# Kernel tuning notes

Measured on AMD Instinct MI355X. Metric: run time of the kernel, lower is better.

The kernel has to match this reference:

```python
import jax, jax.numpy as jnp
import numpy as np

B, N, M = 2, 4096, 1024
QD, CD, H, DH = 512, 768, 8, 64
SCALE = DH ** -0.5


def setup_inputs() -> dict:
    key = jax.random.key(0)
    ks = jax.random.split(key, 8)
    return {
        "x": jax.random.normal(ks[0], (B, N, QD), jnp.float32),
        "context": jax.random.normal(ks[1], (B, M, CD), jnp.float32),
        "adapt": jax.random.normal(ks[2], (B, N, H * DH), jnp.float32),
        "Wq": jax.random.normal(ks[3], (QD, H * DH), jnp.float32) * (QD ** -0.5),
        "Wk": jax.random.normal(ks[4], (CD, H * DH), jnp.float32) * (CD ** -0.5),
        "Wv": jax.random.normal(ks[5], (CD, H * DH), jnp.float32) * (CD ** -0.5),
        "Wo": jax.random.normal(ks[6], (H * DH, QD), jnp.float32) * ((H * DH) ** -0.5),
        "bo": jnp.zeros((QD,), jnp.float32),
    }


def _split_heads(t):
    # [b, n, h*d] -> [b, h, n, d]
    b, n, _ = t.shape
    return t.reshape(b, n, H, DH).transpose(0, 2, 1, 3)


def reference(x, context, adapt, Wq, Wk, Wv, Wo, bo):
    q = _split_heads(x @ Wq)          # [b,h,n,d]
    k = _split_heads(context @ Wk)    # [b,h,m,d]
    v = _split_heads(context @ Wv)    # [b,h,m,d]

    sim = jnp.einsum('bhid,bhjd->bhij', q, k) * SCALE  # [b,h,n,m]
    attn = jax.nn.softmax(sim, axis=-1)
    # NOTE: module averages raw logits (sim) over heads, not softmax probs
    attention_probs_avg = sim.mean(axis=1)             # [b,n,m]
    out = jnp.einsum('bhij,bhjd->bhid', attn, v)       # [b,h,n,d]

    # adapt-query pass reusing k, v
    qa = _split_heads(adapt)
    sim_a = jnp.einsum('bhid,bhjd->bhij', qa, k) * SCALE
    attn_a = jax.nn.softmax(sim_a, axis=-1)
    out = out + jnp.einsum('bhij,bhjd->bhid', attn_a, v)

    out = out.transpose(0, 2, 1, 3).reshape(B, N, H * DH)  # merge heads
    return (out @ Wo + bo, attention_probs_avg)
```

## Files before the change

### kernel.cpp

```cpp
#include <hip/hip_runtime.h>

typedef __attribute__((ext_vector_type(8))) short bh8;
typedef __attribute__((ext_vector_type(4))) float f4;
typedef __attribute__((ext_vector_type(4))) unsigned short us4;
typedef __attribute__((ext_vector_type(4))) unsigned int u32x4;

__device__ __forceinline__ unsigned short rne_bf16(float x) {
  unsigned int u = __builtin_bit_cast(unsigned int, x);
  u += 0x7fffu + ((u >> 16) & 1u);
  return (unsigned short)(u >> 16);
}

__device__ __forceinline__ unsigned int cvt_pk_bf16(float lo, float hi) {
  unsigned int r;
  asm("v_cvt_pk_bf16_f32 %0, %1, %2" : "=v"(r) : "v"(lo), "v"(hi));
  return r;
}

__device__ __forceinline__ void gl_lds16(const void* g, void* l) {
  __builtin_amdgcn_global_load_lds(
      (const __attribute__((address_space(1))) void*)g,
      (__attribute__((address_space(3))) void*)l, 16, 0, 0);
}

__global__ __launch_bounds__(256) void prep_kernel(
    const float* __restrict__ x, unsigned short* __restrict__ xb,
    const float* __restrict__ context, unsigned short* __restrict__ cb,
    const float* __restrict__ Wq, const float* __restrict__ Wk,
    const float* __restrict__ Wv, const float* __restrict__ Wo,
    unsigned short* __restrict__ WqT, unsigned short* __restrict__ WkvT,
    unsigned short* __restrict__ WoT) {
  const int bid = blockIdx.x, tid = threadIdx.x;
  if (bid < 1024) {
    const int n40 = (8192 * 512) / 4, n41 = (2048 * 768) / 4;
    const int total = n40 + n41, stride = 1024 * 256;
    for (int i = bid * 256 + tid; i < total; i += stride) {
      const float* in = (i < n40) ? x : context;
      unsigned short* out = (i < n40) ? xb : cb;
      const int j = (i < n40) ? i : (i - n40);
      f4 v = *(const f4*)(in + (long)j * 4);
      us4 o;
#pragma unroll
      for (int e = 0; e < 4; ++e) o[e] = rne_bf16(v[e]);
      *(us4*)(out + (long)j * 4) = o;
    }
    return;
  }
  int u = bid - 1024;
  const float* in;
  unsigned short* out;
  int K;
  if (u < 256)       { in = Wq; out = WqT;               K = 512; }
  else if (u < 640)  { u -= 256; in = Wk; out = WkvT;    K = 768; }
  else if (u < 1024) { u -= 640; in = Wv; out = WkvT + 512L * 768; K = 768; }
  else               { u -= 1024; in = Wo; out = WoT;    K = 512; }
  const int N = 512;
  const int n0 = (u & 15) * 32, k0 = (u >> 4) * 32;
  __shared__ float t[32][33];
  const int tx = tid & 31, ty = tid >> 5;
#pragma unroll
  for (int r = 0; r < 32; r += 8)
    t[ty + r][tx] = in[(long)(k0 + ty + r) * N + n0 + tx];
  __syncthreads();
#pragma unroll
  for (int r = 0; r < 32; r += 8)
    out[(long)(n0 + ty + r) * K + k0 + tx] = rne_bf16(t[tx][ty + r]);
}

__global__ __launch_bounds__(256) void vt_kernel(
    const unsigned short* __restrict__ KVb, unsigned short* __restrict__ VTb) {
  const int u = blockIdx.x;
  const int j0 = (u & 63) * 32, d0 = (u >> 6) * 32;
  __shared__ unsigned short t[32][34];
  const int tx = threadIdx.x & 31, ty = threadIdx.x >> 5;
#pragma unroll
  for (int r = 0; r < 32; r += 8)
    t[ty + r][tx] = KVb[(long)(j0 + ty + r) * 1024 + 512 + d0 + tx];
  __syncthreads();
#pragma unroll
  for (int r = 0; r < 32; r += 8)
    VTb[(long)(d0 + ty + r) * 2048 + j0 + tx] = t[tx][ty + r];
}

template <int MODE>
__device__ __forceinline__ void gemm_body(
    char* ldsb,
    const unsigned short* __restrict__ A, const unsigned short* __restrict__ Bt,
    void* __restrict__ Cv, int K, int lda, int ldb, int ldc,
    long astr, long bstr, long cstr, float scale, const float* __restrict__ bias,
    int bx, int by, int bz) {
  char* Asb = ldsb;
  char* Bsb = ldsb + 32768;
  const int tid = threadIdx.x, w = tid >> 6, l = tid & 63;
  const int c = l & 15, g = l >> 4;
  const int m0 = by * 128, n0 = bx * 128;
  const unsigned short* Ab = A + (long)bz * astr;
  const unsigned short* Bb = Bt + (long)bz * bstr;

  auto stage = [&](int buf, int kt) {
#pragma unroll
    for (int s = 0; s < 4; ++s) {
      const int idx = w * 4 + s;
      const int row = ((idx >> 1) & 7) * 16 + c;
      const int col = kt * 64 + (idx & 1) * 32 + g * 8;
      gl_lds16(Ab + (long)(m0 + row) * lda + col, Asb + buf * 16384 + idx * 1024);
      gl_lds16(Bb + (long)(n0 + row) * ldb + col, Bsb + buf * 16384 + idx * 1024);
    }
  };

  f4 acc[4][4];
#pragma unroll
  for (int i = 0; i < 4; ++i)
#pragma unroll
    for (int j = 0; j < 4; ++j) acc[i][j] = (f4){0.f, 0.f, 0.f, 0.f};

  const int nkt = K >> 6;
  stage(0, 0);
  asm volatile("s_waitcnt vmcnt(0)" ::: "memory");
  __syncthreads();

  for (int kt = 0; kt < nkt; ++kt) {
    const int cur = kt & 1;
    if (kt + 1 < nkt) stage(cur ^ 1, kt + 1);
#pragma unroll
    for (int kk = 0; kk < 2; ++kk) {
      bh8 af[4], bfr[4];
#pragma unroll
      for (int i = 0; i < 4; ++i) {
        af[i] = *(const bh8*)(Asb + cur * 16384 + (((w >> 1) * 8 + i * 2 + kk) * 1024) + l * 16);
        bfr[i] = *(const bh8*)(Bsb + cur * 16384 + (((w & 1) * 8 + i * 2 + kk) * 1024) + l * 16);
      }
#pragma unroll
      for (int i = 0; i < 4; ++i)
#pragma unroll
        for (int j = 0; j < 4; ++j)
          acc[i][j] = __builtin_amdgcn_mfma_f32_16x16x32_bf16(af[i], bfr[j], acc[i][j], 0, 0, 0);
    }
    if (kt + 1 < nkt) {
      asm volatile("s_waitcnt vmcnt(0)" ::: "memory");
      __syncthreads();
    }
  }

  const int rbase = m0 + (w >> 1) * 64, cbase = n0 + (w & 1) * 64;
#pragma unroll
  for (int i = 0; i < 4; ++i)
#pragma unroll
    for (int j = 0; j < 4; ++j)
#pragma unroll
      for (int r = 0; r < 4; ++r) {
        const long row = rbase + i * 16 + g * 4 + r;
        const long col = cbase + j * 16 + c;
        const float v = acc[i][j][r];
        if (MODE == 0) {
          ((unsigned short*)Cv + (long)bz * cstr)[row * ldc + col] = rne_bf16(v * scale);
        } else if (MODE == 1) {
          ((float*)Cv + (long)bz * cstr)[row * ldc + col] = v * scale;
        } else {
          ((float*)Cv)[row * ldc + col] = v + bias[col];
        }
      }
}

template <int MODE>
__device__ __forceinline__ void gemm_body64(
    char* ldsb,
    const unsigned short* __restrict__ A, const unsigned short* __restrict__ Bt,
    void* __restrict__ Cv, int K, int lda, int ldb, int ldc,
    float scale, const float* __restrict__ bias, int bx, int by) {
  char* Asb = ldsb;
  char* Bsb = ldsb + 32768;
  const int tid = threadIdx.x, w = tid >> 6, l = tid & 63;
  const int c = l & 15, g = l >> 4;
  const int m0 = by * 128, n0 = bx * 64;
  const int wr = w & 1, wc = w >> 1;

  auto stage = [&](int buf, int kt) {
#pragma unroll
    for (int s = 0; s < 6; ++s) {
      const int idx = w * 6 + s;
      if (idx < 16) {
        const int row = (idx >> 1) * 16 + c;
        const int col = kt * 64 + (idx & 1) * 32 + g * 8;
        gl_lds16(A + (long)(m0 + row) * lda + col, Asb + buf * 16384 + idx * 1024);
      } else {
        const int ib = idx - 16;
        const int row = (ib >> 1) * 16 + c;
        const int col = kt * 64 + (ib & 1) * 32 + g * 8;
        gl_lds16(Bt + (long)(n0 + row) * ldb + col, Bsb + buf * 8192 + ib * 1024);
      }
    }
  };

  f4 acc[4][2];
#pragma unroll
  for (int i = 0; i < 4; ++i)
#pragma unroll
    for (int j = 0; j < 2; ++j) acc[i][j] = (f4){0.f, 0.f, 0.f, 0.f};

  const int nkt = K >> 6;
  stage(0, 0);
  asm volatile("s_waitcnt vmcnt(0)" ::: "memory");
  __syncthreads();

  for (int kt = 0; kt < nkt; ++kt) {
    const int cur = kt & 1;
    if (kt + 1 < nkt) stage(cur ^ 1, kt + 1);
#pragma unroll
    for (int kk = 0; kk < 2; ++kk) {
      bh8 af[4], bfr[2];
#pragma unroll
      for (int i = 0; i < 4; ++i)
        af[i] = *(const bh8*)(Asb + cur * 16384 + (((wr * 4 + i) * 2 + kk) * 1024) + l * 16);
#pragma unroll
      for (int j = 0; j < 2; ++j)
        bfr[j] = *(const bh8*)(Bsb + cur * 8192 + (((wc * 2 + j) * 2 + kk) * 1024) + l * 16);
#pragma unroll
      for (int i = 0; i < 4; ++i)
#pragma unroll
        for (int j = 0; j < 2; ++j)
          acc[i][j] = __builtin_amdgcn_mfma_f32_16x16x32_bf16(af[i], bfr[j], acc[i][j], 0, 0, 0);
    }
    if (kt + 1 < nkt) {
      asm volatile("s_waitcnt vmcnt(0)" ::: "memory");
      __syncthreads();
    }
  }

  const int rbase = m0 + wr * 64, cbase = n0 + wc * 32;
#pragma unroll
  for (int i = 0; i < 4; ++i)
#pragma unroll
    for (int j = 0; j < 2; ++j)
#pragma unroll
      for (int r = 0; r < 4; ++r) {
        const long row = rbase + i * 16 + g * 4 + r;
        const long col = cbase + j * 16 + c;
        const float v = acc[i][j][r];
        if (MODE == 0) {
          ((unsigned short*)Cv)[row * ldc + col] = rne_bf16(v * scale);
        } else if (MODE == 2) {
          ((float*)Cv)[row * ldc + col] = v + bias[col];
        }
      }
}

__global__ __launch_bounds__(256, 3) void gemm_qkv(
    const unsigned short* __restrict__ xb, const unsigned short* __restrict__ WqT,
    unsigned short* __restrict__ Qb,
    const unsigned short* __restrict__ cb, const unsigned short* __restrict__ WkvT,
    unsigned short* __restrict__ KVb, float cexp) {
  __shared__ char lds[49152];
  const int bid = blockIdx.x;
  const unsigned short *A, *Bt;
  unsigned short* C;
  int K, ldb_, ldc_, bx, by;
  float sc;
  if (bid < 512) {
    A = xb; Bt = WqT; C = Qb; K = 512; ldb_ = 512; ldc_ = 512;
    bx = bid & 7; by = bid >> 3; sc = cexp;
  } else {
    const int u = bid - 512;
    A = cb; Bt = WkvT; C = KVb; K = 768; ldb_ = 768; ldc_ = 1024;
    bx = u & 15; by = u >> 4; sc = 1.f;
  }
  gemm_body64<0>(lds, A, Bt, C, K, K, ldb_, ldc_, sc, nullptr, bx, by);
}

__global__ __launch_bounds__(256, 2) void final_kernel(
    const unsigned short* __restrict__ Qb, const unsigned short* __restrict__ KVb,
    float* __restrict__ out1, float avg_scale,
    const unsigned short* __restrict__ Ob, const unsigned short* __restrict__ WoT,
    float* __restrict__ out0, const float* __restrict__ bias) {
  extern __shared__ char lds[];
  const int bid = blockIdx.x;
  if (bid < 512) {
    gemm_body<1>(lds, Qb, KVb, out1, 512, 512, 1024, 1024,
                 4096L * 512, 1024L * 1024, 4096L * 1024, avg_scale, nullptr,
                 bid & 7, (bid >> 3) & 31, bid >> 8);
  } else {
    const int u = bid - 512;
    gemm_body64<2>(lds, Ob, WoT, out0, 512, 512, 512, 512, 1.f, bias, u & 7, u >> 3);
  }
}

__global__ __launch_bounds__(256, 4) void attn_kernel(
    const unsigned short* __restrict__ Qb, const float* __restrict__ adapt,
    const unsigned short* __restrict__ KV, const unsigned short* __restrict__ VT,
    unsigned short* __restrict__ Ob) {
  __shared__ unsigned short Ks[2][8 * 512];
  __shared__ unsigned short Vs[2][8 * 512];
  const int qt = blockIdx.y, h = blockIdx.x, b = blockIdx.z;
  const int tid = threadIdx.x, w = tid >> 6, l = tid & 63;
  const int c = l & 15, g = l >> 4;
  const float CEXP = 0.18033688011112042f;

  const unsigned short* Kg = KV + ((long)b * 1024) * 1024 + h * 64;
  const unsigned short* Vg = VT + (long)h * 64 * 2048 + b * 1024;

  auto stage = [&](int buf, int jt0) {
#pragma unroll
    for (int s = 0; s < 2; ++s) {
      const int idx = w * 2 + s;
      const int row = (idx >> 1) * 16 + c;
      const int col = (idx & 1) * 32 + g * 8;
      gl_lds16(Kg + ((long)jt0 * 64 + row) * 1024 + col, (char*)&Ks[buf][0] + idx * 1024);
      gl_lds16(Vg + (long)row * 2048 + jt0 * 64 + col, (char*)&Vs[buf][0] + idx * 1024);
    }
  };

  stage(0, 0);

  const long qrow = (long)b * 4096 + qt * 64 + w * 16 + c;
  bh8 qf[2][2];
#pragma unroll
  for (int kk = 0; kk < 2; ++kk) {
    const int col = h * 64 + kk * 32 + g * 8;
    qf[0][kk] = *(const bh8*)(Qb + qrow * 512 + col);
    const float* ap = adapt + qrow * 512 + col;
    f4 x0 = *(const f4*)ap, x1 = *(const f4*)(ap + 4);
    bh8 t;
#pragma unroll
    for (int e = 0; e < 4; ++e) {
      t[e] = (short)rne_bf16(x0[e] * CEXP);
      t[e + 4] = (short)rne_bf16(x1[e] * CEXP);
    }
    qf[1][kk] = t;
  }

  const u32x4 ones_u = {0x3F803F80u, 0x3F803F80u, 0x3F803F80u, 0x3F803F80u};
  const bh8 ones = __builtin_bit_cast(bh8, ones_u);

  f4 psacc[2];
  f4 accv[2][4];
#pragma unroll
  for (int qs = 0; qs < 2; ++qs) {
    psacc[qs] = (f4){0.f, 0.f, 0.f, 0.f};
#pragma unroll
    for (int dt = 0; dt < 4; ++dt) accv[qs][dt] = (f4){0.f, 0.f, 0.f, 0.f};
  }

  asm volatile("s_waitcnt vmcnt(0)" ::: "memory");
  __syncthreads();

  auto make_pf = [&](const f4& s2k, const f4& s2k1) -> bh8 {
    unsigned int p0 = cvt_pk_bf16(s2k[0], s2k[1]);
    unsigned int p1 = cvt_pk_bf16(s2k[2], s2k[3]);
    unsigned int q0 = cvt_pk_bf16(s2k1[0], s2k1[1]);
    unsigned int q1 = cvt_pk_bf16(s2k1[2], s2k1[3]);
    asm("v_permlane32_swap_b32 %0, %1" : "+v"(p0), "+v"(q0));
    asm("v_permlane16_swap_b32 %0, %1" : "+v"(p0), "+v"(q0));
    asm("v_permlane32_swap_b32 %0, %1" : "+v"(p1), "+v"(q1));
    asm("v_permlane16_swap_b32 %0, %1" : "+v"(p1), "+v"(q1));
    u32x4 u = {p0, p1, q0, q1};
    return __builtin_bit_cast(bh8, u);
  };

  for (int jt0 = 0; jt0 < 16; ++jt0) {
    const int cur = jt0 & 1;
    if (jt0 < 15) stage(cur ^ 1, jt0 + 1);

    f4 s0[4], s1[4];
    __builtin_amdgcn_s_setprio(1);
#pragma unroll
    for (int jt = 0; jt < 4; ++jt) {
      bh8 k0 = *(const bh8*)((const char*)&Ks[cur][0] + (jt * 2 + 0) * 1024 + l * 16);
      bh8 k1 = *(const bh8*)((const char*)&Ks[cur][0] + (jt * 2 + 1) * 1024 + l * 16);
      s0[jt] = (f4){0.f, 0.f, 0.f, 0.f};
      s0[jt] = __builtin_amdgcn_mfma_f32_16x16x32_bf16(k0, qf[0][0], s0[jt], 0, 0, 0);
      s0[jt] = __builtin_amdgcn_mfma_f32_16x16x32_bf16(k1, qf[0][1], s0[jt], 0, 0, 0);
      s1[jt] = (f4){0.f, 0.f, 0.f, 0.f};
      s1[jt] = __builtin_amdgcn_mfma_f32_16x16x32_bf16(k0, qf[1][0], s1[jt], 0, 0, 0);
      s1[jt] = __builtin_amdgcn_mfma_f32_16x16x32_bf16(k1, qf[1][1], s1[jt], 0, 0, 0);
    }
    __builtin_amdgcn_s_setprio(0);

#pragma unroll
    for (int jt = 0; jt < 4; ++jt)
#pragma unroll
      for (int r = 0; r < 4; ++r) {
        s0[jt][r] = __builtin_amdgcn_exp2f(s0[jt][r]);
        s1[jt][r] = __builtin_amdgcn_exp2f(s1[jt][r]);
      }

    bh8 pf0[2], pf1[2];
#pragma unroll
    for (int kk = 0; kk < 2; ++kk) {
      pf0[kk] = make_pf(s0[2 * kk], s0[2 * kk + 1]);
      pf1[kk] = make_pf(s1[2 * kk], s1[2 * kk + 1]);
    }

    bh8 vf[4][2];
#pragma unroll
    for (int dt = 0; dt < 4; ++dt)
#pragma unroll
      for (int kk = 0; kk < 2; ++kk)
        vf[dt][kk] = *(const bh8*)((const char*)&Vs[cur][0] + (dt * 2 + kk) * 1024 + l * 16);

    psacc[0] = __builtin_amdgcn_mfma_f32_16x16x32_bf16(ones, pf0[0], psacc[0], 0, 0, 0);
    psacc[0] = __builtin_amdgcn_mfma_f32_16x16x32_bf16(ones, pf0[1], psacc[0], 0, 0, 0);
    psacc[1] = __builtin_amdgcn_mfma_f32_16x16x32_bf16(ones, pf1[0], psacc[1], 0, 0, 0);
    psacc[1] = __builtin_amdgcn_mfma_f32_16x16x32_bf16(ones, pf1[1], psacc[1], 0, 0, 0);

    __builtin_amdgcn_s_setprio(1);
#pragma unroll
    for (int dt = 0; dt < 4; ++dt) {
      accv[0][dt] = __builtin_amdgcn_mfma_f32_16x16x32_bf16(vf[dt][0], pf0[0], accv[0][dt], 0, 0, 0);
      accv[0][dt] = __builtin_amdgcn_mfma_f32_16x16x32_bf16(vf[dt][1], pf0[1], accv[0][dt], 0, 0, 0);
      accv[1][dt] = __builtin_amdgcn_mfma_f32_16x16x32_bf16(vf[dt][0], pf1[0], accv[1][dt], 0, 0, 0);
      accv[1][dt] = __builtin_amdgcn_mfma_f32_16x16x32_bf16(vf[dt][1], pf1[1], accv[1][dt], 0, 0, 0);
    }
    __builtin_amdgcn_s_setprio(0);

    if (jt0 < 15) {
      asm volatile("s_waitcnt vmcnt(0)" ::: "memory");
      __syncthreads();
    }
  }

  const float i0 = 1.0f / psacc[0][0], i1 = 1.0f / psacc[1][0];
  const long orow = (long)b * 4096 + qt * 64 + w * 16 + c;
#pragma unroll
  for (int dt = 0; dt < 4; ++dt) {
    float v0 = accv[0][dt][0] * i0 + accv[1][dt][0] * i1;
    float v1 = accv[0][dt][1] * i0 + accv[1][dt][1] * i1;
    float v2 = accv[0][dt][2] * i0 + accv[1][dt][2] * i1;
    float v3 = accv[0][dt][3] * i0 + accv[1][dt][3] * i1;
    uint2 o;
    o.x = cvt_pk_bf16(v0, v1);
    o.y = cvt_pk_bf16(v2, v3);
    *(uint2*)(Ob + orow * 512 + h * 64 + dt * 16 + g * 4) = o;
  }
}

extern "C" void kernel_launch(void* const* d_in, const int* in_sizes, int n_in,
                              void* d_out, int out_size, void* d_ws, size_t ws_size,
                              hipStream_t stream) {
  (void)in_sizes; (void)n_in; (void)out_size; (void)ws_size;
  const float* x       = (const float*)d_in[0];
  const float* context = (const float*)d_in[1];
  const float* adapt   = (const float*)d_in[2];
  const float* Wq      = (const float*)d_in[3];
  const float* Wk      = (const float*)d_in[4];
  const float* Wv      = (const float*)d_in[5];
  const float* Wo      = (const float*)d_in[6];
  const float* bo      = (const float*)d_in[7];
  float* out0 = (float*)d_out;
  float* out1 = out0 + (long)2 * 4096 * 512;

  const float CEXP = 0.18033688011112042f;
  const float AVG_SCALE = 0.015625f / CEXP;

  char* wp = (char*)d_ws;
  auto take = [&](long elems) { unsigned short* p = (unsigned short*)wp; wp += elems * 2; return p; };
  unsigned short* xb   = take(8192L * 512);
  unsigned short* cb   = take(2048L * 768);
  unsigned short* WqT  = take(512L * 512);
  unsigned short* WkvT = take(1024L * 768);
  unsigned short* WoT  = take(512L * 512);
  unsigned short* Qb   = take(8192L * 512);
  unsigned short* KVb  = take(2048L * 1024);
  unsigned short* VTb  = take(512L * 2048);
  unsigned short* Ob   = take(8192L * 512);

  prep_kernel<<<2304, 256, 0, stream>>>(x, xb, context, cb, Wq, Wk, Wv, Wo, WqT, WkvT, WoT);
  gemm_qkv<<<768, 256, 0, stream>>>(xb, WqT, Qb, cb, WkvT, KVb, CEXP);
  vt_kernel<<<1024, 256, 0, stream>>>(KVb, VTb);
  attn_kernel<<<dim3(8, 64, 2), 256, 0, stream>>>(Qb, adapt, KVb, VTb, Ob);
  final_kernel<<<1024, 256, 65536, stream>>>(Qb, KVb, out1, AVG_SCALE, Ob, WoT, out0, bo);
}
```

Before: 117.3 us.

## Split attention query streams across separate waves with LDS combine

The attention kernel now runs 512 threads per block. Each pair of waves handles the same 16 query rows, one wave doing the x-query pass and the other the adapt-query pass, instead of one wave doing both. This halves per-wave register state (accumulators, score tiles, V fragments), which should allow more resident waves and more latency hiding. In exchange, the two partial outputs are combined through LDS scratch with an extra barrier at the end, and each wave now loads one staging chunk instead of two.

```diff
diff --git a/kernel.cpp b/kernel.cpp
--- a/kernel.cpp
+++ b/kernel.cpp
@@ -284,7 +284,7 @@
   }
 }
 
-__global__ __launch_bounds__(256, 4) void attn_kernel(
+__global__ __launch_bounds__(512, 6) void attn_kernel(
     const unsigned short* __restrict__ Qb, const float* __restrict__ adapt,
     const unsigned short* __restrict__ KV, const unsigned short* __restrict__ VT,
     unsigned short* __restrict__ Ob) {
@@ -293,52 +293,48 @@
   const int qt = blockIdx.y, h = blockIdx.x, b = blockIdx.z;
   const int tid = threadIdx.x, w = tid >> 6, l = tid & 63;
   const int c = l & 15, g = l >> 4;
+  const int qs = w & 1, p = w >> 1;
   const float CEXP = 0.18033688011112042f;
 
   const unsigned short* Kg = KV + ((long)b * 1024) * 1024 + h * 64;
   const unsigned short* Vg = VT + (long)h * 64 * 2048 + b * 1024;
 
   auto stage = [&](int buf, int jt0) {
-#pragma unroll
-    for (int s = 0; s < 2; ++s) {
-      const int idx = w * 2 + s;
-      const int row = (idx >> 1) * 16 + c;
-      const int col = (idx & 1) * 32 + g * 8;
-      gl_lds16(Kg + ((long)jt0 * 64 + row) * 1024 + col, (char*)&Ks[buf][0] + idx * 1024);
-      gl_lds16(Vg + (long)row * 2048 + jt0 * 64 + col, (char*)&Vs[buf][0] + idx * 1024);
-    }
+    const int row = (w >> 1) * 16 + c;
+    const int col = (w & 1) * 32 + g * 8;
+    gl_lds16(Kg + ((long)jt0 * 64 + row) * 1024 + col, (char*)&Ks[buf][0] + w * 1024);
+    gl_lds16(Vg + (long)row * 2048 + jt0 * 64 + col, (char*)&Vs[buf][0] + w * 1024);
   };
 
   stage(0, 0);
 
-  const long qrow = (long)b * 4096 + qt * 64 + w * 16 + c;
-  bh8 qf[2][2];
+  const long qrow = (long)b * 4096 + qt * 64 + p * 16 + c;
+  bh8 qf[2];
 #pragma unroll
   for (int kk = 0; kk < 2; ++kk) {
     const int col = h * 64 + kk * 32 + g * 8;
-    qf[0][kk] = *(const bh8*)(Qb + qrow * 512 + col);
-    const float* ap = adapt + qrow * 512 + col;
-    f4 x0 = *(const f4*)ap, x1 = *(const f4*)(ap + 4);
-    bh8 t;
-#pragma unroll
-    for (int e = 0; e < 4; ++e) {
-      t[e] = (short)rne_bf16(x0[e] * CEXP);
-      t[e + 4] = (short)rne_bf16(x1[e] * CEXP);
-    }
-    qf[1][kk] = t;
+    if (qs == 0) {
+      qf[kk] = *(const bh8*)(Qb + qrow * 512 + col);
+    } else {
+      const float* ap = adapt + qrow * 512 + col;
+      f4 x0 = *(const f4*)ap, x1 = *(const f4*)(ap + 4);
+      bh8 t;
+#pragma unroll
+      for (int e = 0; e < 4; ++e) {
+        t[e] = (short)rne_bf16(x0[e] * CEXP);
+        t[e + 4] = (short)rne_bf16(x1[e] * CEXP);
+      }
+      qf[kk] = t;
+    }
   }
 
   const u32x4 ones_u = {0x3F803F80u, 0x3F803F80u, 0x3F803F80u, 0x3F803F80u};
   const bh8 ones = __builtin_bit_cast(bh8, ones_u);
 
-  f4 psacc[2];
-  f4 accv[2][4];
-#pragma unroll
-  for (int qs = 0; qs < 2; ++qs) {
-    psacc[qs] = (f4){0.f, 0.f, 0.f, 0.f};
-#pragma unroll
-    for (int dt = 0; dt < 4; ++dt) accv[qs][dt] = (f4){0.f, 0.f, 0.f, 0.f};
-  }
+  f4 psacc = (f4){0.f, 0.f, 0.f, 0.f};
+  f4 accv[4];
+#pragma unroll
+  for (int dt = 0; dt < 4; ++dt) accv[dt] = (f4){0.f, 0.f, 0.f, 0.f};
 
   asm volatile("s_waitcnt vmcnt(0)" ::: "memory");
   __syncthreads();
@@ -360,55 +356,39 @@
     const int cur = jt0 & 1;
     if (jt0 < 15) stage(cur ^ 1, jt0 + 1);
 
-    f4 s0[4], s1[4];
+    f4 s[4];
     __builtin_amdgcn_s_setprio(1);
 #pragma unroll
     for (int jt = 0; jt < 4; ++jt) {
       bh8 k0 = *(const bh8*)((const char*)&Ks[cur][0] + (jt * 2 + 0) * 1024 + l * 16);
       bh8 k1 = *(const bh8*)((const char*)&Ks[cur][0] + (jt * 2 + 1) * 1024 + l * 16);
-      s0[jt] = (f4){0.f, 0.f, 0.f, 0.f};
-      s0[jt] = __builtin_amdgcn_mfma_f32_16x16x32_bf16(k0, qf[0][0], s0[jt], 0, 0, 0);
-      s0[jt] = __builtin_amdgcn_mfma_f32_16x16x32_bf16(k1, qf[0][1], s0[jt], 0, 0, 0);
-      s1[jt] = (f4){0.f, 0.f, 0.f, 0.f};
-      s1[jt] = __builtin_amdgcn_mfma_f32_16x16x32_bf16(k0, qf[1][0], s1[jt], 0, 0, 0);
-      s1[jt] = __builtin_amdgcn_mfma_f32_16x16x32_bf16(k1, qf[1][1], s1[jt], 0, 0, 0);
+      s[jt] = (f4){0.f, 0.f, 0.f, 0.f};
+      s[jt] = __builtin_amdgcn_mfma_f32_16x16x32_bf16(k0, qf[0], s[jt], 0, 0, 0);
+      s[jt] = __builtin_amdgcn_mfma_f32_16x16x32_bf16(k1, qf[1], s[jt], 0, 0, 0);
     }
     __builtin_amdgcn_s_setprio(0);
 
 #pragma unroll
     for (int jt = 0; jt < 4; ++jt)
 #pragma unroll
-      for (int r = 0; r < 4; ++r) {
-        s0[jt][r] = __builtin_amdgcn_exp2f(s0[jt][r]);
-        s1[jt][r] = __builtin_amdgcn_exp2f(s1[jt][r]);
-      }
-
-    bh8 pf0[2], pf1[2];
-#pragma unroll
-    for (int kk = 0; kk < 2; ++kk) {
-      pf0[kk] = make_pf(s0[2 * kk], s0[2 * kk + 1]);
-      pf1[kk] = make_pf(s1[2 * kk], s1[2 * kk + 1]);
-    }
-
-    bh8 vf[4][2];
-#pragma unroll
-    for (int dt = 0; dt < 4; ++dt)
-#pragma unroll
-      for (int kk = 0; kk < 2; ++kk)
-        vf[dt][kk] = *(const bh8*)((const char*)&Vs[cur][0] + (dt * 2 + kk) * 1024 + l * 16);
-
-    psacc[0] = __builtin_amdgcn_mfma_f32_16x16x32_bf16(ones, pf0[0], psacc[0], 0, 0, 0);
-    psacc[0] = __builtin_amdgcn_mfma_f32_16x16x32_bf16(ones, pf0[1], psacc[0], 0, 0, 0);
-    psacc[1] = __builtin_amdgcn_mfma_f32_16x16x32_bf16(ones, pf1[0], psacc[1], 0, 0, 0);
-    psacc[1] = __builtin_amdgcn_mfma_f32_16x16x32_bf16(ones, pf1[1], psacc[1], 0, 0, 0);
+      for (int r = 0; r < 4; ++r)
+        s[jt][r] = __builtin_amdgcn_exp2f(s[jt][r]);
+
+    bh8 pf[2];
+#pragma unroll
+    for (int kk = 0; kk < 2; ++kk)
+      pf[kk] = make_pf(s[2 * kk], s[2 * kk + 1]);
+
+    psacc = __builtin_amdgcn_mfma_f32_16x16x32_bf16(ones, pf[0], psacc, 0, 0, 0);
+    psacc = __builtin_amdgcn_mfma_f32_16x16x32_bf16(ones, pf[1], psacc, 0, 0, 0);
 
     __builtin_amdgcn_s_setprio(1);
 #pragma unroll
     for (int dt = 0; dt < 4; ++dt) {
-      accv[0][dt] = __builtin_amdgcn_mfma_f32_16x16x32_bf16(vf[dt][0], pf0[0], accv[0][dt], 0, 0, 0);
-      accv[0][dt] = __builtin_amdgcn_mfma_f32_16x16x32_bf16(vf[dt][1], pf0[1], accv[0][dt], 0, 0, 0);
-      accv[1][dt] = __builtin_amdgcn_mfma_f32_16x16x32_bf16(vf[dt][0], pf1[0], accv[1][dt], 0, 0, 0);
-      accv[1][dt] = __builtin_amdgcn_mfma_f32_16x16x32_bf16(vf[dt][1], pf1[1], accv[1][dt], 0, 0, 0);
+      bh8 v0 = *(const bh8*)((const char*)&Vs[cur][0] + (dt * 2 + 0) * 1024 + l * 16);
+      bh8 v1 = *(const bh8*)((const char*)&Vs[cur][0] + (dt * 2 + 1) * 1024 + l * 16);
+      accv[dt] = __builtin_amdgcn_mfma_f32_16x16x32_bf16(v0, pf[0], accv[dt], 0, 0, 0);
+      accv[dt] = __builtin_amdgcn_mfma_f32_16x16x32_bf16(v1, pf[1], accv[dt], 0, 0, 0);
     }
     __builtin_amdgcn_s_setprio(0);
 
@@ -418,18 +398,31 @@
     }
   }
 
-  const float i0 = 1.0f / psacc[0][0], i1 = 1.0f / psacc[1][0];
-  const long orow = (long)b * 4096 + qt * 64 + w * 16 + c;
-#pragma unroll
-  for (int dt = 0; dt < 4; ++dt) {
-    float v0 = accv[0][dt][0] * i0 + accv[1][dt][0] * i1;
-    float v1 = accv[0][dt][1] * i0 + accv[1][dt][1] * i1;
-    float v2 = accv[0][dt][2] * i0 + accv[1][dt][2] * i1;
-    float v3 = accv[0][dt][3] * i0 + accv[1][dt][3] * i1;
-    uint2 o;
-    o.x = cvt_pk_bf16(v0, v1);
-    o.y = cvt_pk_bf16(v2, v3);
-    *(uint2*)(Ob + orow * 512 + h * 64 + dt * 16 + g * 4) = o;
+  __syncthreads();
+  float* scratch = (p < 2) ? (float*)&Ks[0][0] + p * 1024
+                           : (float*)&Vs[0][0] + (p - 2) * 1024;
+  const float inv = 1.0f / psacc[0];
+  if (qs == 1) {
+#pragma unroll
+    for (int dt = 0; dt < 4; ++dt) {
+      f4 v = accv[dt] * inv;
+      const int colb = (dt * 16 + g * 4 + c * 4) & 63;
+      *(f4*)(scratch + c * 64 + colb) = v;
+    }
+  }
+  __syncthreads();
+  if (qs == 0) {
+    const long orow = (long)b * 4096 + qt * 64 + p * 16 + c;
+#pragma unroll
+    for (int dt = 0; dt < 4; ++dt) {
+      const int colb = (dt * 16 + g * 4 + c * 4) & 63;
+      f4 other = *(const f4*)(scratch + c * 64 + colb);
+      f4 v = accv[dt] * inv + other;
+      uint2 o;
+      o.x = cvt_pk_bf16(v[0], v[1]);
+      o.y = cvt_pk_bf16(v[2], v[3]);
+      *(uint2*)(Ob + orow * 512 + h * 64 + dt * 16 + g * 4) = o;
+    }
   }
 }
 
@@ -466,6 +459,6 @@
   prep_kernel<<<2304, 256, 0, stream>>>(x, xb, context, cb, Wq, Wk, Wv, Wo, WqT, WkvT, WoT);
   gemm_qkv<<<768, 256, 0, stream>>>(xb, WqT, Qb, cb, WkvT, KVb, CEXP);
   vt_kernel<<<1024, 256, 0, stream>>>(KVb, VTb);
-  attn_kernel<<<dim3(8, 64, 2), 256, 0, stream>>>(Qb, adapt, KVb, VTb, Ob);
+  attn_kernel<<<dim3(8, 64, 2), 512, 0, stream>>>(Qb, adapt, KVb, VTb, Ob);
   final_kernel<<<1024, 256, 65536, stream>>>(Qb, KVb, out1, AVG_SCALE, Ob, WoT, out0, bo);
 }
```

After: 127.2 us. +8.5%, slower.
